# Optimization experiments

Measured on AMD Instinct MI355X. Metric: run time of the kernel, lower is better.

## Reference

```python
import jax, jax.numpy as jnp
import numpy as np

PATCH_SIZE = 14
MERGE = 2  # spatial_merge_size
D = 1024
B = 8
IMG_PX = 1792  # 128 patches per side


def setup_inputs() -> dict:
    key = jax.random.key(0)
    k1, k2 = jax.random.split(key)
    n_patches_per_img = (IMG_PX // PATCH_SIZE) ** 2  # 16384
    total = B * n_patches_per_img                    # 131072
    image_features = jax.random.normal(k1, (1, total, D), dtype=jnp.float32)
    image_sizes = jnp.full((B, 2), IMG_PX, dtype=jnp.int32)
    # nn.Linear(D*MERGE**2, D, bias=False): weight (D, D*MERGE**2), y = x @ W.T
    W = jax.random.normal(k2, (D, D * MERGE * MERGE), dtype=jnp.float32) * (1.0 / np.sqrt(D * MERGE * MERGE))
    return {"image_features": image_features, "image_sizes": image_sizes, "W": W}


def _merge_one(xi, h, w, S):
    # xi: (h*w, D) in row-major (h, w) patch order
    d = xi.shape[-1]
    x = xi.reshape(h // S, S, w // S, S, d)
    # -> (h/S, w/S, D, S, S): matches torch unfold channel-major (d, ki, kj) column order
    x = x.transpose(0, 2, 4, 1, 3)
    return x.reshape((h // S) * (w // S), d * S * S)


def reference(image_features, image_sizes, W):
    sizes = np.asarray(image_sizes)  # static per-image pixel sizes
    x = image_features[0]  # (sum N_i, D)
    S = MERGE
    blocks = []
    off = 0
    for h_px, w_px in sizes:  # loop over B images (small, structurally distinct shapes)
        h, w = int(h_px) // PATCH_SIZE, int(w_px) // PATCH_SIZE
        n = h * w
        blocks.append(_merge_one(jax.lax.dynamic_slice_in_dim(x, off, n, axis=0), h, w, S))
        off += n
    merged = jnp.concatenate(blocks, axis=0)            # (sum L_i, D*S^2)
    out = jnp.einsum('nk,dk->nd', merged, W)            # single global GEMM
    return out[None, :, :]                              # (1, sum L_i, D)
```

## Files before the change

kernel.cpp:

```cpp
#include <hip/hip_runtime.h>
#include <hip/hip_bf16.h>
#include <stdint.h>


#define M_TOTAL 32768
#define K_DIM   4096
#define N_DIM   1024
#define BM 128
#define BN 128
#define BK 64

typedef __attribute__((ext_vector_type(8))) short short8;
typedef __attribute__((ext_vector_type(4))) float f32x4;
typedef __attribute__((ext_vector_type(8))) unsigned short us8;

#define ASYNC_COPY16(gsrc, ldst)                                                     \
    __builtin_amdgcn_global_load_lds(                                                \
        (const __attribute__((address_space(1))) unsigned int*)(const void*)(gsrc),  \
        (__attribute__((address_space(3))) unsigned int*)(ldst), 16, 0, 0)

static __device__ __forceinline__ unsigned pack2bf(float lo, float hi) {
    unsigned a = __builtin_bit_cast(unsigned, lo) + 0x8000u;
    unsigned b = __builtin_bit_cast(unsigned, hi) + 0x8000u;
    return __builtin_amdgcn_perm(b, a, 0x07060302);
}

__global__ __launch_bounds__(256) void repack_w(const float* __restrict__ W,
                                                unsigned short* __restrict__ Wp) {
    int t = blockIdx.x * 256 + threadIdx.x;
    int j  = t >> 8;
    int d0 = (t & 255) << 2;
    const float4* src = (const float4*)(W + (size_t)j * K_DIM + (size_t)d0 * 4);
    float4 v0 = src[0], v1 = src[1], v2 = src[2], v3 = src[3];
    float vs[4][4] = {{v0.x, v1.x, v2.x, v3.x},
                      {v0.y, v1.y, v2.y, v3.y},
                      {v0.z, v1.z, v2.z, v3.z},
                      {v0.w, v1.w, v2.w, v3.w}};
#pragma unroll
    for (int s = 0; s < 4; s++) {
        uint2 o;
        o.x = pack2bf(vs[s][0], vs[s][1]);
        o.y = pack2bf(vs[s][2], vs[s][3]);
        *(uint2*)(Wp + (size_t)j * K_DIM + s * 1024 + d0) = o;
    }
}

__global__ __launch_bounds__(256) void gather_convert(const float* __restrict__ X,
                                                      unsigned short* __restrict__ Ap) {
    int idx = blockIdx.x * 256 + threadIdx.x;
    int p   = idx >> 6;
    int c16 = (idx & 63) << 4;
    int img = p >> 14;
    int r   = p & 16383;
    int pi  = r >> 7;
    int pj  = r & 127;
    int m   = img * 4096 + (pi >> 1) * 64 + (pj >> 1);
    int s   = ((pi & 1) << 1) | (pj & 1);
    const float4* src = (const float4*)(X + (size_t)p * 1024 + c16);
    float4 v0 = src[0], v1 = src[1], v2 = src[2], v3 = src[3];
    uint4 o0, o1;
    o0.x = pack2bf(v0.x, v0.y); o0.y = pack2bf(v0.z, v0.w);
    o0.z = pack2bf(v1.x, v1.y); o0.w = pack2bf(v1.z, v1.w);
    o1.x = pack2bf(v2.x, v2.y); o1.y = pack2bf(v2.z, v2.w);
    o1.z = pack2bf(v3.x, v3.y); o1.w = pack2bf(v3.z, v3.w);
    uint4* dst = (uint4*)(Ap + (size_t)m * K_DIM + s * 1024 + c16);
    dst[0] = o0;
    dst[1] = o1;
}

#define NT 32

#define SBAR() do { asm volatile("" ::: "memory");            \
                    __builtin_amdgcn_s_barrier();             \
                    asm volatile("" ::: "memory"); } while (0)
#define WAITLG()  asm volatile("s_waitcnt lgkmcnt(0)" ::: "memory")
#define WAITVM6() asm volatile("s_waitcnt vmcnt(6)" ::: "memory")

__global__ __launch_bounds__(512, 2) void gemm_8p(
        const unsigned short* __restrict__ Ap,
        const unsigned short* __restrict__ Wp,
        float* __restrict__ out) {
    __shared__ unsigned short lds[2][2][2][8192];

    const int tid  = threadIdx.x;
    const int lane = tid & 63;
    const int wave = tid >> 6;
    const int wr   = wave >> 2;
    const int wc   = wave & 3;
    const int lrow = lane & 15;
    const int quad = lane >> 4;

    const int bid = blockIdx.x;
    const int lw  = (bid & 7) * 64 + (bid >> 3);
    const int bn  = (lw & 3) * 256;
    const int bm  = (lw >> 2) * 256;

    const int rho   = lane >> 2;
    const int kappa = (lane & 3) ^ ((lane >> 5) << 1);
    const int r128s = wave * 16 + rho;
    const unsigned short* aptr[2];
    const unsigned short* bptr[2];
#pragma unroll
    for (int h = 0; h < 2; h++) {
        const int ra = ((r128s >> 6) << 7) + h * 64 + (r128s & 63);
        const int rb = ((r128s >> 5) << 6) + h * 32 + (r128s & 31);
        aptr[h] = Ap + (size_t)(bm + ra) * K_DIM + kappa * 8;
        bptr[h] = Wp + (size_t)(bn + rb) * K_DIM + kappa * 8;
    }

#define STAGE_A(slot, h, kt) do {                                                 \
    ASYNC_COPY16(aptr[h] + (kt) * 64,      &lds[slot][0][h][wave * 1024]);        \
    ASYNC_COPY16(aptr[h] + (kt) * 64 + 32, &lds[slot][0][h][wave * 1024 + 512]);  \
} while (0)
#define STAGE_B(slot, h, kt) do {                                                 \
    ASYNC_COPY16(bptr[h] + (kt) * 64,      &lds[slot][1][h][wave * 1024]);        \
    ASYNC_COPY16(bptr[h] + (kt) * 64 + 32, &lds[slot][1][h][wave * 1024 + 512]);  \
} while (0)

    const int rswz = (lrow * 64 + quad * 16) ^ ((lrow & 8) << 2);
    short8 a[4][2], b0[2][2], b1[2][2];
    f32x4 acc[8][4] = {};

#define LDA(slot, mh) do {                                                        \
    const char* base_ = (const char*)&lds[slot][0][mh][0] + rswz;                 \
    _Pragma("unroll") for (int ii = 0; ii < 4; ii++)                              \
    _Pragma("unroll") for (int kk = 0; kk < 2; kk++)                              \
        a[ii][kk] = *(const short8*)(base_ + (wr * 4 + ii) * 2048 + kk * 1024);   \
} while (0)
#define LDB(slot, nh, breg) do {                                                  \
    const char* base_ = (const char*)&lds[slot][1][nh][0] + rswz;                 \
    _Pragma("unroll") for (int jj = 0; jj < 2; jj++)                              \
    _Pragma("unroll") for (int kk = 0; kk < 2; kk++)                              \
        breg[jj][kk] = *(const short8*)(base_ + (wc * 2 + jj) * 2048 + kk * 1024);\
} while (0)
#define MMA(mh, nh, breg) do {                                                    \
    _Pragma("unroll") for (int ii = 0; ii < 4; ii++)                              \
    _Pragma("unroll") for (int jj = 0; jj < 2; jj++)                              \
    _Pragma("unroll") for (int kk = 0; kk < 2; kk++)                              \
        acc[(mh) * 4 + ii][(nh) * 2 + jj] =                                       \
            __builtin_amdgcn_mfma_f32_16x16x32_bf16(                              \
                a[ii][kk], breg[jj][kk], acc[(mh) * 4 + ii][(nh) * 2 + jj],       \
                0, 0, 0);                                                         \
} while (0)

    STAGE_B(0, 0, 0); STAGE_A(0, 0, 0); STAGE_B(0, 1, 0); STAGE_A(0, 1, 0);
    STAGE_B(1, 0, 1); STAGE_A(1, 0, 1); STAGE_B(1, 1, 1);
    WAITVM6();
    SBAR();

#pragma unroll 1
    for (int t = 0; t < NT; t++) {
        const int ko = 2 * t + 1;
        const int ne = (2 * t + 2) & 63;
        const int no = (2 * t + 3) & 63;

        LDA(0, 0); LDB(0, 0, b0);
        STAGE_A(1, 1, ko);
        SBAR(); WAITLG();
        __builtin_amdgcn_s_setprio(1); MMA(0, 0, b0); __builtin_amdgcn_s_setprio(0);
        SBAR();
        LDB(0, 1, b1);
        STAGE_B(0, 0, ne);
        SBAR(); WAITLG();
        __builtin_amdgcn_s_setprio(1); MMA(0, 1, b1); __builtin_amdgcn_s_setprio(0);
        SBAR();
        LDA(0, 1);
        STAGE_A(0, 0, ne);
        SBAR(); WAITLG();
        __builtin_amdgcn_s_setprio(1); MMA(1, 0, b0); __builtin_amdgcn_s_setprio(0);
        SBAR();
        STAGE_B(0, 1, ne);
        SBAR();
        __builtin_amdgcn_s_setprio(1); MMA(1, 1, b1); __builtin_amdgcn_s_setprio(0);
        WAITVM6();
        SBAR();
        LDA(1, 0); LDB(1, 0, b0);
        STAGE_A(0, 1, ne);
        SBAR(); WAITLG();
        __builtin_amdgcn_s_setprio(1); MMA(0, 0, b0); __builtin_amdgcn_s_setprio(0);
        SBAR();
        LDB(1, 1, b1);
        STAGE_B(1, 0, no);
        SBAR(); WAITLG();
        __builtin_amdgcn_s_setprio(1); MMA(0, 1, b1); __builtin_amdgcn_s_setprio(0);
        SBAR();
        LDA(1, 1);
        STAGE_A(1, 0, no);
        SBAR(); WAITLG();
        __builtin_amdgcn_s_setprio(1); MMA(1, 0, b0); __builtin_amdgcn_s_setprio(0);
        SBAR();
        STAGE_B(1, 1, no);
        SBAR();
        __builtin_amdgcn_s_setprio(1); MMA(1, 1, b1); __builtin_amdgcn_s_setprio(0);
        WAITVM6();
        SBAR();
    }

    asm volatile("s_waitcnt vmcnt(0)" ::: "memory");

    const int ocol = bn + wc * 64 + lrow;
#pragma unroll
    for (int i = 0; i < 8; i++) {
#pragma unroll
        for (int r = 0; r < 4; r++) {
            float* po = out + (size_t)(bm + wr * 128 + i * 16 + quad * 4 + r) * N_DIM + ocol;
#pragma unroll
            for (int j = 0; j < 4; j++)
                po[j * 16] = acc[i][j][r];
        }
    }
}

#define LP 72
__global__ __launch_bounds__(256) void merge_gemm(
        const float* __restrict__ X,
        const unsigned short* __restrict__ Wp,
        float* __restrict__ out) {
    __shared__ unsigned short As[BM][LP];
    __shared__ unsigned short Bs[BN][LP];

    const int tid  = threadIdx.x;
    const int lane = tid & 63;
    const int wave = tid >> 6;
    const int wm   = (wave >> 1) * 64;
    const int wn   = (wave & 1) * 64;
    const int lrow = lane & 15;
    const int quad = lane >> 4;

    const int blk = blockIdx.x;
    const int bn  = (blk & 7) * BN;
    const int bm  = (blk >> 3) * BM;

    const int arow = tid >> 4;
    const int acol = (tid & 15) << 2;

    const float* abase[8];
#pragma unroll
    for (int rep = 0; rep < 8; rep++) {
        int m   = bm + arow + rep * 16;
        int img = m >> 12;
        int r   = m & 4095;
        int bi  = r >> 6;
        int bj  = r & 63;
        int pbase = img * 16384 + bi * 256 + bj * 2;
        abase[rep] = X + (size_t)pbase * 1024 + acol;
    }

    const int brow = tid >> 3;
    const int bcol = (tid & 7) << 3;

    f32x4 acc[4][4] = {};

    for (int k0 = 0; k0 < K_DIM; k0 += BK) {
        const int s    = k0 >> 10;
        const int d0   = k0 & 1023;
        const int aoff = (((s >> 1) * 128) + (s & 1)) * 1024 + d0;

#pragma unroll
        for (int rep = 0; rep < 8; rep++) {
            const float4 v = *(const float4*)(abase[rep] + aoff);
            uint2 o;
            o.x = pack2bf(v.x, v.y);
            o.y = pack2bf(v.z, v.w);
            *(uint2*)&As[arow + rep * 16][acol] = o;
        }
#pragma unroll
        for (int rep = 0; rep < 4; rep++) {
            us8 v = *(const us8*)(Wp + (size_t)(bn + brow + rep * 32) * K_DIM + k0 + bcol);
            *(us8*)&Bs[brow + rep * 32][bcol] = v;
        }
        __syncthreads();

#pragma unroll
        for (int kk = 0; kk < 2; kk++) {
            const int koff = kk * 32 + quad * 8;
            short8 a[4], b[4];
#pragma unroll
            for (int i = 0; i < 4; i++)
                a[i] = *(const short8*)&As[wm + i * 16 + lrow][koff];
#pragma unroll
            for (int j = 0; j < 4; j++)
                b[j] = *(const short8*)&Bs[wn + j * 16 + lrow][koff];
#pragma unroll
            for (int i = 0; i < 4; i++)
#pragma unroll
                for (int j = 0; j < 4; j++)
                    acc[i][j] = __builtin_amdgcn_mfma_f32_16x16x32_bf16(
                        a[i], b[j], acc[i][j], 0, 0, 0);
        }
        __syncthreads();
    }

    const int ocol = bn + wn + lrow;
#pragma unroll
    for (int i = 0; i < 4; i++) {
#pragma unroll
        for (int r = 0; r < 4; r++) {
            float* po = out + (size_t)(bm + wm + i * 16 + quad * 4 + r) * N_DIM + ocol;
#pragma unroll
            for (int j = 0; j < 4; j++)
                po[j * 16] = acc[i][j][r];
        }
    }
}

extern "C" void kernel_launch(void* const* d_in, const int* in_sizes, int n_in,
                              void* d_out, int out_size, void* d_ws, size_t ws_size,
                              hipStream_t stream) {
    const float* X = (const float*)d_in[0];
    const float* W = (const float*)d_in[2];
    float* out = (float*)d_out;

    unsigned short* Wp = (unsigned short*)d_ws;
    const size_t WP_BYTES = (size_t)N_DIM * K_DIM * 2;
    const size_t AP_BYTES = (size_t)M_TOTAL * K_DIM * 2;

    repack_w<<<dim3(1024), dim3(256), 0, stream>>>(W, Wp);

    if (ws_size >= WP_BYTES + AP_BYTES) {
        unsigned short* Ap = (unsigned short*)((char*)d_ws + WP_BYTES);
        gather_convert<<<dim3(32768), dim3(256), 0, stream>>>(X, Ap);
        gemm_8p<<<dim3(512), dim3(512), 0, stream>>>(Ap, Wp, out);
    } else {
        merge_gemm<<<dim3((M_TOTAL / BM) * (N_DIM / BN)), dim3(256), 0, stream>>>(X, Wp, out);
    }
}
```

Before: 964.9 us.

## Double-buffer A fragments in registers to overlap LDS reads with MFMA

Adds a second A register buffer and moves each LDS fragment load one phase earlier, so the next sub-tile's reads are issued before the current MFMA block runs. The MMA order becomes (0,0),(1,0),(0,1),(1,1), and vmcnt waits are relaxed to vmcnt(2) at new points. sched_barrier calls keep the compiler from reordering loads across MFMA groups. The aim is to hide LDS latency behind matrix math, at the cost of more VGPR pressure that could hurt occupancy at 512 threads with 2 blocks per CU, plus a risk of race hazards from the changed wait placement.

```diff
diff --git a/kernel.cpp b/kernel.cpp
--- a/kernel.cpp
+++ b/kernel.cpp
@@ -74,7 +74,11 @@
                     __builtin_amdgcn_s_barrier();             \
                     asm volatile("" ::: "memory"); } while (0)
 #define WAITLG()  asm volatile("s_waitcnt lgkmcnt(0)" ::: "memory")
+#define WAITVM2() asm volatile("s_waitcnt vmcnt(2)" ::: "memory")
 #define WAITVM6() asm volatile("s_waitcnt vmcnt(6)" ::: "memory")
+#define SCHED0()  __builtin_amdgcn_sched_barrier(0)
+#define PRIO1()   __builtin_amdgcn_s_setprio(1)
+#define PRIO0()   __builtin_amdgcn_s_setprio(0)
 
 __global__ __launch_bounds__(512, 2) void gemm_8p(
         const unsigned short* __restrict__ Ap,
@@ -118,28 +122,28 @@
 } while (0)
 
     const int rswz = (lrow * 64 + quad * 16) ^ ((lrow & 8) << 2);
-    short8 a[4][2], b0[2][2], b1[2][2];
+    short8 aP[4][2], aQ[4][2], b0[2][2], b1[2][2];
     f32x4 acc[8][4] = {};
 
-#define LDA(slot, mh) do {                                                        \
+#define LDA_R(dst, slot, mh) do {                                                 \
     const char* base_ = (const char*)&lds[slot][0][mh][0] + rswz;                 \
     _Pragma("unroll") for (int ii = 0; ii < 4; ii++)                              \
     _Pragma("unroll") for (int kk = 0; kk < 2; kk++)                              \
-        a[ii][kk] = *(const short8*)(base_ + (wr * 4 + ii) * 2048 + kk * 1024);   \
-} while (0)
-#define LDB(slot, nh, breg) do {                                                  \
+        dst[ii][kk] = *(const short8*)(base_ + (wr * 4 + ii) * 2048 + kk * 1024); \
+} while (0)
+#define LDB_R(dst, slot, nh) do {                                                 \
     const char* base_ = (const char*)&lds[slot][1][nh][0] + rswz;                 \
     _Pragma("unroll") for (int jj = 0; jj < 2; jj++)                              \
     _Pragma("unroll") for (int kk = 0; kk < 2; kk++)                              \
-        breg[jj][kk] = *(const short8*)(base_ + (wc * 2 + jj) * 2048 + kk * 1024);\
-} while (0)
-#define MMA(mh, nh, breg) do {                                                    \
+        dst[jj][kk] = *(const short8*)(base_ + (wc * 2 + jj) * 2048 + kk * 1024); \
+} while (0)
+#define MMA(mh, nh, areg, breg) do {                                              \
     _Pragma("unroll") for (int ii = 0; ii < 4; ii++)                              \
     _Pragma("unroll") for (int jj = 0; jj < 2; jj++)                              \
     _Pragma("unroll") for (int kk = 0; kk < 2; kk++)                              \
         acc[(mh) * 4 + ii][(nh) * 2 + jj] =                                       \
             __builtin_amdgcn_mfma_f32_16x16x32_bf16(                              \
-                a[ii][kk], breg[jj][kk], acc[(mh) * 4 + ii][(nh) * 2 + jj],       \
+                areg[ii][kk], breg[jj][kk], acc[(mh) * 4 + ii][(nh) * 2 + jj],    \
                 0, 0, 0);                                                         \
 } while (0)
 
@@ -147,6 +151,7 @@
     STAGE_B(1, 0, 1); STAGE_A(1, 0, 1); STAGE_B(1, 1, 1);
     WAITVM6();
     SBAR();
+    LDA_R(aP, 0, 0); LDB_R(b0, 0, 0);
 
 #pragma unroll 1
     for (int t = 0; t < NT; t++) {
@@ -154,49 +159,59 @@
         const int ne = (2 * t + 2) & 63;
         const int no = (2 * t + 3) & 63;
 
-        LDA(0, 0); LDB(0, 0, b0);
         STAGE_A(1, 1, ko);
-        SBAR(); WAITLG();
-        __builtin_amdgcn_s_setprio(1); MMA(0, 0, b0); __builtin_amdgcn_s_setprio(0);
-        SBAR();
-        LDB(0, 1, b1);
+        SBAR(); WAITLG(); SCHED0();
+        LDA_R(aQ, 0, 1);
+        SCHED0();
+        PRIO1(); MMA(0, 0, aP, b0); PRIO0();
+        SBAR();
         STAGE_B(0, 0, ne);
-        SBAR(); WAITLG();
-        __builtin_amdgcn_s_setprio(1); MMA(0, 1, b1); __builtin_amdgcn_s_setprio(0);
-        SBAR();
-        LDA(0, 1);
+        SBAR(); WAITLG(); SCHED0();
+        LDB_R(b1, 0, 1);
+        SCHED0();
+        PRIO1(); MMA(1, 0, aQ, b0); PRIO0();
+        WAITVM2();
+        SBAR();
         STAGE_A(0, 0, ne);
-        SBAR(); WAITLG();
-        __builtin_amdgcn_s_setprio(1); MMA(1, 0, b0); __builtin_amdgcn_s_setprio(0);
+        SBAR(); WAITLG(); SCHED0();
+        LDB_R(b0, 1, 0);
+        SCHED0();
+        PRIO1(); MMA(0, 1, aP, b1); PRIO0();
         SBAR();
         STAGE_B(0, 1, ne);
-        SBAR();
-        __builtin_amdgcn_s_setprio(1); MMA(1, 1, b1); __builtin_amdgcn_s_setprio(0);
-        WAITVM6();
-        SBAR();
-        LDA(1, 0); LDB(1, 0, b0);
+        SBAR(); WAITLG(); SCHED0();
+        LDA_R(aP, 1, 0);
+        SCHED0();
+        PRIO1(); MMA(1, 1, aQ, b1); PRIO0();
+        SBAR();
         STAGE_A(0, 1, ne);
-        SBAR(); WAITLG();
-        __builtin_amdgcn_s_setprio(1); MMA(0, 0, b0); __builtin_amdgcn_s_setprio(0);
-        SBAR();
-        LDB(1, 1, b1);
+        SBAR(); WAITLG(); SCHED0();
+        LDA_R(aQ, 1, 1);
+        SCHED0();
+        PRIO1(); MMA(0, 0, aP, b0); PRIO0();
+        SBAR();
         STAGE_B(1, 0, no);
-        SBAR(); WAITLG();
-        __builtin_amdgcn_s_setprio(1); MMA(0, 1, b1); __builtin_amdgcn_s_setprio(0);
-        SBAR();
-        LDA(1, 1);
+        SBAR(); WAITLG(); SCHED0();
+        LDB_R(b1, 1, 1);
+        SCHED0();
+        PRIO1(); MMA(1, 0, aQ, b0); PRIO0();
+        WAITVM2();
+        SBAR();
         STAGE_A(1, 0, no);
-        SBAR(); WAITLG();
-        __builtin_amdgcn_s_setprio(1); MMA(1, 0, b0); __builtin_amdgcn_s_setprio(0);
+        SBAR(); WAITLG(); SCHED0();
+        LDB_R(b0, 0, 0);
+        SCHED0();
+        PRIO1(); MMA(0, 1, aP, b1); PRIO0();
         SBAR();
         STAGE_B(1, 1, no);
-        SBAR();
-        __builtin_amdgcn_s_setprio(1); MMA(1, 1, b1); __builtin_amdgcn_s_setprio(0);
-        WAITVM6();
-        SBAR();
-    }
-
-    asm volatile("s_waitcnt vmcnt(0)" ::: "memory");
+        SBAR(); WAITLG(); SCHED0();
+        LDA_R(aP, 0, 0);
+        SCHED0();
+        PRIO1(); MMA(1, 1, aQ, b1); PRIO0();
+        SBAR();
+    }
+
+    asm volatile("s_waitcnt vmcnt(0) lgkmcnt(0)" ::: "memory");
 
     const int ocol = bn + wc * 64 + lrow;
 #pragma unroll
```

Result: no change. 956.2 us (-0.9%).
